# Optimization experiments

Hardware: AMD Instinct MI355X
Metric: run time of the kernel (lower is better)

Reference implementation:

```python
import jax, jax.numpy as jnp
import numpy as np

N, E = 65536, 524288
IN_DIM, HID_DIM, OUT_DIM = 1024, 512, 256


def setup_inputs() -> dict:
    key = jax.random.key(0)
    k1, k2, k3, k4, k5, k6 = jax.random.split(key, 6)
    h = jax.random.normal(k1, (N, IN_DIM), dtype=jnp.float32)
    src = jax.random.randint(k2, (E,), 0, N, dtype=jnp.int64)
    dst = jax.random.randint(k3, (E,), 0, N, dtype=jnp.int64)
    # Glorot-uniform weights as in DGL GraphConv
    lim1 = float(np.sqrt(6.0 / (IN_DIM + HID_DIM)))
    lim2 = float(np.sqrt(6.0 / (HID_DIM + OUT_DIM)))
    W1 = jax.random.uniform(k4, (IN_DIM, HID_DIM), jnp.float32, -lim1, lim1)
    W2 = jax.random.uniform(k5, (HID_DIM, OUT_DIM), jnp.float32, -lim2, lim2)
    b1 = jnp.zeros((HID_DIM,), jnp.float32)
    b2 = jnp.zeros((OUT_DIM,), jnp.float32)
    return {"h": h, "W1": W1, "b1": b1, "W2": W2, "b2": b2, "src": src, "dst": dst}


def _graph_conv(x, W, b, src, dst, inv_sqrt_dout, inv_sqrt_din):
    # DGL GraphConv, norm='both': D_in^{-1/2} A D_out^{-1/2} X W + b
    # Apply dense transform first (in_dim >= out_dim path in DGL) -- same math.
    x = x * inv_sqrt_dout[:, None]
    x = x @ W  # [N, out]
    agg = jax.ops.segment_sum(x[src], dst, num_segments=x.shape[0])  # scatter-add over edges
    return agg * inv_sqrt_din[:, None] + b


def reference(h, W1, b1, W2, b2, src, dst):
    n = h.shape[0]
    ones = jnp.ones((src.shape[0],), h.dtype)
    deg_out = jnp.maximum(jax.ops.segment_sum(ones, src, num_segments=n), 1.0)
    deg_in = jnp.maximum(jax.ops.segment_sum(ones, dst, num_segments=n), 1.0)
    inv_sqrt_dout = jax.lax.rsqrt(deg_out)
    inv_sqrt_din = jax.lax.rsqrt(deg_in)
    x = _graph_conv(h, W1, b1, src, dst, inv_sqrt_dout, inv_sqrt_din)
    x = jax.nn.elu(x)  # act; dropout p=0 -> identity
    out = _graph_conv(x, W2, b2, src, dst, inv_sqrt_dout, inv_sqrt_din)
    return out  # last_act = Identity
```

## Files before the change

### kernel.cpp

```cpp
#include <hip/hip_runtime.h>
#include <hip/hip_bf16.h>

#define IN_DIM 1024
#define HID 512
#define OUTD 256

typedef __attribute__((ext_vector_type(8))) short short8;
typedef __attribute__((ext_vector_type(4))) float f32x4;
typedef __attribute__((ext_vector_type(8))) unsigned short ushort8e;
typedef __attribute__((ext_vector_type(4))) unsigned short ushort4e;

template<int F> struct VecSel;
template<> struct VecSel<8> { using T = ushort8e; };
template<> struct VecSel<4> { using T = ushort4e; };


__device__ inline unsigned short f2bf(float f) {
    union { float f; unsigned u; } v; v.f = f;
    unsigned r = (v.u + 0x7FFF + ((v.u >> 16) & 1)) >> 16;
    return (unsigned short)r;
}

__device__ inline float bf2f(unsigned short u) {
    union { unsigned u; float f; } v; v.u = ((unsigned)u) << 16; return v.f;
}

__device__ inline void gload16(const void* g, void* l) {
    __builtin_amdgcn_global_load_lds(
        (const __attribute__((address_space(1))) void*)g,
        (__attribute__((address_space(3))) void*)l, 16, 0, 0);
}


__global__ void deg_kernel(const int* __restrict__ src, const int* __restrict__ dst,
                           int* __restrict__ dego, int* __restrict__ degi, int E) {
    int i = blockIdx.x * blockDim.x + threadIdx.x;
    if (i < E) {
        atomicAdd(&dego[src[i]], 1);
        atomicAdd(&degi[dst[i]], 1);
    }
}

__global__ void invsqrt_kernel(const int* __restrict__ dego, const int* __restrict__ degi,
                               float* __restrict__ iso, float* __restrict__ isi, int n) {
    int i = blockIdx.x * blockDim.x + threadIdx.x;
    if (i < n) {
        iso[i] = rsqrtf(fmaxf((float)dego[i], 1.0f));
        isi[i] = rsqrtf(fmaxf((float)degi[i], 1.0f));
    }
}


__global__ __launch_bounds__(256) void scan_block(const int* __restrict__ deg,
                                                  int* __restrict__ excl,
                                                  int* __restrict__ partials) {
    __shared__ int tmp[256];
    int tid = threadIdx.x;
    int i = blockIdx.x * 256 + tid;
    int v = deg[i];
    tmp[tid] = v;
    __syncthreads();
    #pragma unroll
    for (int off = 1; off < 256; off <<= 1) {
        int t = (tid >= off) ? tmp[tid - off] : 0;
        __syncthreads();
        tmp[tid] += t;
        __syncthreads();
    }
    excl[i] = tmp[tid] - v;
    if (tid == 255) partials[blockIdx.x] = tmp[255];
}

__global__ __launch_bounds__(256) void scan_partials(int* __restrict__ partials) {
    __shared__ int tmp[256];
    int tid = threadIdx.x;
    int v = partials[tid];
    tmp[tid] = v;
    __syncthreads();
    #pragma unroll
    for (int off = 1; off < 256; off <<= 1) {
        int t = (tid >= off) ? tmp[tid - off] : 0;
        __syncthreads();
        tmp[tid] += t;
        __syncthreads();
    }
    partials[tid] = tmp[tid] - v;
}

__global__ __launch_bounds__(256) void scan_add(const int* __restrict__ excl,
                                                const int* __restrict__ partials,
                                                const int* __restrict__ deg,
                                                int* __restrict__ row_start,
                                                int* __restrict__ cursor, int n) {
    int i = blockIdx.x * 256 + threadIdx.x;
    int v = excl[i] + partials[blockIdx.x];
    row_start[i] = v;
    cursor[i] = v;
    if (i == n - 1) row_start[n] = v + deg[i];
}

__global__ void csr_fill(const int* __restrict__ src, const int* __restrict__ dst,
                         int* __restrict__ cursor, int* __restrict__ eidx, int E) {
    int e = blockIdx.x * blockDim.x + threadIdx.x;
    if (e < E) {
        int pos = atomicAdd(&cursor[dst[e]], 1);
        eidx[pos] = src[e];
    }
}


__global__ void transpose_cvt(const float* __restrict__ W, unsigned short* __restrict__ Wt,
                              int K, int N) {
    int i = blockIdx.x * 256 + threadIdx.x;
    if (i < N * K) {
        int n = i / K, k = i - n * K;
        Wt[i] = f2bf(W[(size_t)k * N + n]);
    }
}


#define TM 128
#define TN 128
#define TK 64
#define NXCD 8

template<int AF32>
__global__ __launch_bounds__(256) void gemm_bf16_mfma(
    const void* __restrict__ Ap, const unsigned short* __restrict__ Bt,
    const float* __restrict__ rowscale, unsigned short* __restrict__ Cb,
    int M, int K, int Nc)
{
    __shared__ unsigned short As[2][TM][TK];
    __shared__ unsigned short Bs[2][TN][TK];

    const int tid  = threadIdx.x;
    const int lane = tid & 63;
    const int wave = tid >> 6;
    const int wr = wave >> 1, wc = wave & 1;
    const int lrow = lane & 15;
    const int lkg  = lane >> 4;

    const int nwg = gridDim.x;
    const int per = nwg / NXCD;
    const int lin = blockIdx.x;
    const int newlin = (lin % NXCD) * per + lin / NXCD;
    const int ncb = Nc / TN;
    const int m0 = (newlin / ncb) * TM;
    const int n0 = (newlin % ncb) * TN;

    int srow[4], sq[4];
    #pragma unroll
    for (int i = 0; i < 4; ++i) {
        int s = i * 256 + wave * 64 + lane;
        srow[i] = s >> 3;
        sq[i] = (s & 7) ^ ((s >> 3) & 7);
    }

    char* AsB = (char*)&As[0][0][0];
    char* BsB = (char*)&Bs[0][0][0];

    const float* Af = (const float*)Ap;
    const unsigned short* Ab = (const unsigned short*)Ap;

    auto stageOp = [&](const unsigned short* G, int rc0, int kt, char* opBase, int buf) {
        const int k0 = kt * TK;
        #pragma unroll
        for (int i = 0; i < 4; ++i)
            gload16(G + (size_t)(rc0 + srow[i]) * K + k0 + sq[i] * 8,
                    opBase + buf * 16384 + (i * 256 + wave * 64) * 16);
    };

    const int rA = tid >> 2;
    const int g  = tid & 3;
    const int qp0 = (2 * g) ^ (rA & 7);
    const int qp1 = (2 * g + 1) ^ (rA & 7);
    float sc0 = 1.f, sc1 = 1.f;
    if (AF32) {
        sc0 = rowscale[m0 + rA];
        sc1 = rowscale[m0 + rA + 64];
    }
    float4 L[8];
    auto loadA = [&](int kt) {
        const float* p0 = Af + (size_t)(m0 + rA) * K + kt * TK + g * 16;
        const float* p1 = p0 + (size_t)64 * K;
        L[0] = *reinterpret_cast<const float4*>(p0);
        L[1] = *reinterpret_cast<const float4*>(p0 + 4);
        L[2] = *reinterpret_cast<const float4*>(p0 + 8);
        L[3] = *reinterpret_cast<const float4*>(p0 + 12);
        L[4] = *reinterpret_cast<const float4*>(p1);
        L[5] = *reinterpret_cast<const float4*>(p1 + 4);
        L[6] = *reinterpret_cast<const float4*>(p1 + 8);
        L[7] = *reinterpret_cast<const float4*>(p1 + 12);
    };
    auto writeA = [&](int buf) {
        short8 k0v, k1v;
        #pragma unroll
        for (int r = 0; r < 2; ++r) {
            const float sc = r ? sc1 : sc0;
            const float4 f0 = L[r * 4 + 0], f1 = L[r * 4 + 1];
            const float4 f2 = L[r * 4 + 2], f3 = L[r * 4 + 3];
            k0v[0] = (short)f2bf(f0.x * sc); k0v[1] = (short)f2bf(f0.y * sc);
            k0v[2] = (short)f2bf(f0.z * sc); k0v[3] = (short)f2bf(f0.w * sc);
            k0v[4] = (short)f2bf(f1.x * sc); k0v[5] = (short)f2bf(f1.y * sc);
            k0v[6] = (short)f2bf(f1.z * sc); k0v[7] = (short)f2bf(f1.w * sc);
            k1v[0] = (short)f2bf(f2.x * sc); k1v[1] = (short)f2bf(f2.y * sc);
            k1v[2] = (short)f2bf(f2.z * sc); k1v[3] = (short)f2bf(f2.w * sc);
            k1v[4] = (short)f2bf(f3.x * sc); k1v[5] = (short)f2bf(f3.y * sc);
            k1v[6] = (short)f2bf(f3.z * sc); k1v[7] = (short)f2bf(f3.w * sc);
            char* rowb = AsB + buf * 16384 + (rA + r * 64) * 128;
            *reinterpret_cast<short8*>(rowb + qp0 * 16) = k0v;
            *reinterpret_cast<short8*>(rowb + qp1 * 16) = k1v;
        }
    };

    f32x4 acc[4][4] = {};

    stageOp(Bt, n0, 0, BsB, 0);
    if (AF32) { loadA(0); writeA(0); }
    else       stageOp(Ab, m0, 0, AsB, 0);
    __syncthreads();

    const int nk = K / TK;
    for (int kt = 0; kt < nk; ++kt) {
        const int cur = kt & 1, nxt = cur ^ 1;

        if (kt + 1 < nk) {
            stageOp(Bt, n0, kt + 1, BsB, nxt);
            if (AF32) loadA(kt + 1);
            else      stageOp(Ab, m0, kt + 1, AsB, nxt);
        }

        #pragma unroll
        for (int ks = 0; ks < 2; ++ks) {
            short8 af[4], bfr[4];
            #pragma unroll
            for (int mi = 0; mi < 4; ++mi) {
                const int row = wr * 64 + mi * 16 + lrow;
                const int qp = (ks * 4 + lkg) ^ (lrow & 7);
                af[mi] = *reinterpret_cast<const short8*>(&As[cur][row][qp * 8]);
            }
            #pragma unroll
            for (int ni = 0; ni < 4; ++ni) {
                const int row = wc * 64 + ni * 16 + lrow;
                const int qp = (ks * 4 + lkg) ^ (lrow & 7);
                bfr[ni] = *reinterpret_cast<const short8*>(&Bs[cur][row][qp * 8]);
            }
            #pragma unroll
            for (int mi = 0; mi < 4; ++mi)
                #pragma unroll
                for (int ni = 0; ni < 4; ++ni)
                    acc[mi][ni] = __builtin_amdgcn_mfma_f32_16x16x32_bf16(
                        af[mi], bfr[ni], acc[mi][ni], 0, 0, 0);
        }

        if (AF32 && kt + 1 < nk) writeA(nxt);

        __syncthreads();
    }

    #pragma unroll
    for (int mi = 0; mi < 4; ++mi)
        #pragma unroll
        for (int ni = 0; ni < 4; ++ni)
            #pragma unroll
            for (int r = 0; r < 4; ++r)
                Cb[(size_t)(m0 + wr * 64 + mi * 16 + (lane >> 4) * 4 + r) * Nc
                   + (n0 + wc * 64 + ni * 16 + lrow)] = f2bf(acc[mi][ni][r]);
}


template<int DIM, bool LAYER1>
__global__ __launch_bounds__(256) void aggregate(
    const int* __restrict__ row_start, const int* __restrict__ eidx,
    const unsigned short* __restrict__ Xb, const float* __restrict__ isi,
    const float* __restrict__ iso, const float* __restrict__ bias,
    unsigned short* __restrict__ out_bf, float* __restrict__ out_f)
{
    constexpr int F = DIM / 64;
    using VecT = typename VecSel<F>::T;
    const int node = blockIdx.x * 4 + (threadIdx.x >> 6);
    const int lane = threadIdx.x & 63;

    const int beg = row_start[node];
    const int end = row_start[node + 1];
    const unsigned short* base = Xb + lane * F;

    float acc[F] = {};
    int e = beg;
    for (; e + 1 < end; e += 2) {
        int i0 = eidx[e], i1 = eidx[e + 1];
        VecT v0 = *reinterpret_cast<const VecT*>(base + (size_t)i0 * DIM);
        VecT v1 = *reinterpret_cast<const VecT*>(base + (size_t)i1 * DIM);
        #pragma unroll
        for (int f = 0; f < F; ++f) { acc[f] += bf2f(v0[f]); acc[f] += bf2f(v1[f]); }
    }
    if (e < end) {
        VecT v0 = *reinterpret_cast<const VecT*>(base + (size_t)eidx[e] * DIM);
        #pragma unroll
        for (int f = 0; f < F; ++f) acc[f] += bf2f(v0[f]);
    }

    const float si = isi[node];
    float bv[F];
    #pragma unroll
    for (int q = 0; q < F / 4; ++q)
        *reinterpret_cast<float4*>(&bv[q * 4]) =
            *reinterpret_cast<const float4*>(bias + lane * F + q * 4);

    if (LAYER1) {
        const float so = iso[node];
        short8 o;
        #pragma unroll
        for (int f = 0; f < F; ++f) {
            float v = acc[f] * si + bv[f];
            v = v > 0.f ? v : expm1f(v);
            o[f] = (short)f2bf(v * so);
        }
        *reinterpret_cast<short8*>(out_bf + (size_t)node * DIM + lane * F) = o;
    } else {
        #pragma unroll
        for (int q = 0; q < F / 4; ++q) {
            float4 v = make_float4(acc[q * 4 + 0] * si + bv[q * 4 + 0],
                                   acc[q * 4 + 1] * si + bv[q * 4 + 1],
                                   acc[q * 4 + 2] * si + bv[q * 4 + 2],
                                   acc[q * 4 + 3] * si + bv[q * 4 + 3]);
            *reinterpret_cast<float4*>(out_f + (size_t)node * DIM + lane * F + q * 4) = v;
        }
    }
}


extern "C" void kernel_launch(void* const* d_in, const int* in_sizes, int n_in,
                              void* d_out, int out_size, void* d_ws, size_t ws_size,
                              hipStream_t stream) {
    const float* h  = (const float*)d_in[0];
    const float* W1 = (const float*)d_in[1];
    const float* b1 = (const float*)d_in[2];
    const float* W2 = (const float*)d_in[3];
    const float* b2 = (const float*)d_in[4];
    const int*   src = (const int*)d_in[5];
    const int*   dst = (const int*)d_in[6];

    const int N = in_sizes[0] / IN_DIM;
    const int E = in_sizes[5];
    float* out = (float*)d_out;

    int* dego      = (int*)d_ws;
    int* degi      = dego + N;
    int* excl      = degi + N;
    int* partials  = excl + N;
    int* row_start = partials + 256;
    int* cursor    = row_start + N + 64;
    int* eidx      = cursor + N;
    float* iso     = (float*)(eidx + E);
    float* isi     = iso + N;
    unsigned short* W1t = (unsigned short*)(isi + N);
    unsigned short* W2t = W1t + (size_t)IN_DIM * HID;
    unsigned short* X1b = W2t + (size_t)HID * OUTD;
    unsigned short* X2b = X1b;
    unsigned short* R2h = X1b + (size_t)N * HID;

    hipMemsetAsync(dego, 0, sizeof(int) * (size_t)2 * N, stream);

    deg_kernel<<<(E + 255) / 256, 256, 0, stream>>>(src, dst, dego, degi, E);
    invsqrt_kernel<<<(N + 255) / 256, 256, 0, stream>>>(dego, degi, iso, isi, N);

    scan_block<<<N / 256, 256, 0, stream>>>(degi, excl, partials);
    scan_partials<<<1, 256, 0, stream>>>(partials);
    scan_add<<<N / 256, 256, 0, stream>>>(excl, partials, degi, row_start, cursor, N);
    csr_fill<<<(E + 255) / 256, 256, 0, stream>>>(src, dst, cursor, eidx, E);

    transpose_cvt<<<(IN_DIM * HID + 255) / 256, 256, 0, stream>>>(W1, W1t, IN_DIM, HID);
    transpose_cvt<<<(HID * OUTD + 255) / 256, 256, 0, stream>>>(W2, W2t, HID, OUTD);

    gemm_bf16_mfma<1><<<(N / TM) * (HID / TN), 256, 0, stream>>>(
        h, W1t, iso, X1b, N, IN_DIM, HID);
    aggregate<HID, true><<<N / 4, 256, 0, stream>>>(
        row_start, eidx, X1b, isi, iso, b1, R2h, nullptr);

    gemm_bf16_mfma<0><<<(N / TM) * (OUTD / TN), 256, 0, stream>>>(
        R2h, W2t, nullptr, X2b, N, HID, OUTD);
    aggregate<OUTD, false><<<N / 4, 256, 0, stream>>>(
        row_start, eidx, X2b, isi, iso, b2, nullptr, out);
}
```

Before: 399.4 us.

## Move layer-1 out-degree scaling from GEMM A-load into edge aggregation

Stops scaling rows of h by inv_sqrt(deg_out) while converting A to bf16 inside the first GEMM. The aggregation kernel instead multiplies each gathered source row by that node's iso value. The change also replaces the manual per-element bf16 rounding with packed hardware conversion and unrolls the gather loop to four edges. This takes multiplies off the GEMM's conversion path, at the cost of an extra scalar gather per edge in aggregation. Rounding changes slightly because the scale is now applied after the bf16 GEMM rather than before it.

```diff
diff --git a/kernel.cpp b/kernel.cpp
--- a/kernel.cpp
+++ b/kernel.cpp
@@ -9,6 +9,7 @@
 typedef __attribute__((ext_vector_type(4))) float f32x4;
 typedef __attribute__((ext_vector_type(8))) unsigned short ushort8e;
 typedef __attribute__((ext_vector_type(4))) unsigned short ushort4e;
+typedef __attribute__((ext_vector_type(4))) unsigned int uint4e;
 
 template<int F> struct VecSel;
 template<> struct VecSel<8> { using T = ushort8e; };
@@ -23,6 +24,11 @@
 
 __device__ inline float bf2f(unsigned short u) {
     union { unsigned u; float f; } v; v.u = ((unsigned)u) << 16; return v.f;
+}
+
+__device__ inline unsigned pkbf(float a, float b) {
+    __hip_bfloat162 h = __float22bfloat162_rn(float2{a, b});
+    union { __hip_bfloat162 h; unsigned u; } v; v.h = h; return v.u;
 }
 
 __device__ inline void gload16(const void* g, void* l) {
@@ -127,8 +133,7 @@
 template<int AF32>
 __global__ __launch_bounds__(256) void gemm_bf16_mfma(
     const void* __restrict__ Ap, const unsigned short* __restrict__ Bt,
-    const float* __restrict__ rowscale, unsigned short* __restrict__ Cb,
-    int M, int K, int Nc)
+    unsigned short* __restrict__ Cb, int M, int K, int Nc)
 {
     __shared__ unsigned short As[2][TM][TK];
     __shared__ unsigned short Bs[2][TN][TK];
@@ -174,11 +179,6 @@
     const int g  = tid & 3;
     const int qp0 = (2 * g) ^ (rA & 7);
     const int qp1 = (2 * g + 1) ^ (rA & 7);
-    float sc0 = 1.f, sc1 = 1.f;
-    if (AF32) {
-        sc0 = rowscale[m0 + rA];
-        sc1 = rowscale[m0 + rA + 64];
-    }
     float4 L[8];
     auto loadA = [&](int kt) {
         const float* p0 = Af + (size_t)(m0 + rA) * K + kt * TK + g * 16;
@@ -193,23 +193,18 @@
         L[7] = *reinterpret_cast<const float4*>(p1 + 12);
     };
     auto writeA = [&](int buf) {
-        short8 k0v, k1v;
         #pragma unroll
         for (int r = 0; r < 2; ++r) {
-            const float sc = r ? sc1 : sc0;
             const float4 f0 = L[r * 4 + 0], f1 = L[r * 4 + 1];
             const float4 f2 = L[r * 4 + 2], f3 = L[r * 4 + 3];
-            k0v[0] = (short)f2bf(f0.x * sc); k0v[1] = (short)f2bf(f0.y * sc);
-            k0v[2] = (short)f2bf(f0.z * sc); k0v[3] = (short)f2bf(f0.w * sc);
-            k0v[4] = (short)f2bf(f1.x * sc); k0v[5] = (short)f2bf(f1.y * sc);
-            k0v[6] = (short)f2bf(f1.z * sc); k0v[7] = (short)f2bf(f1.w * sc);
-            k1v[0] = (short)f2bf(f2.x * sc); k1v[1] = (short)f2bf(f2.y * sc);
-            k1v[2] = (short)f2bf(f2.z * sc); k1v[3] = (short)f2bf(f2.w * sc);
-            k1v[4] = (short)f2bf(f3.x * sc); k1v[5] = (short)f2bf(f3.y * sc);
-            k1v[6] = (short)f2bf(f3.z * sc); k1v[7] = (short)f2bf(f3.w * sc);
+            uint4e a, b;
+            a[0] = pkbf(f0.x, f0.y); a[1] = pkbf(f0.z, f0.w);
+            a[2] = pkbf(f1.x, f1.y); a[3] = pkbf(f1.z, f1.w);
+            b[0] = pkbf(f2.x, f2.y); b[1] = pkbf(f2.z, f2.w);
+            b[2] = pkbf(f3.x, f3.y); b[3] = pkbf(f3.z, f3.w);
             char* rowb = AsB + buf * 16384 + (rA + r * 64) * 128;
-            *reinterpret_cast<short8*>(rowb + qp0 * 16) = k0v;
-            *reinterpret_cast<short8*>(rowb + qp1 * 16) = k1v;
+            *reinterpret_cast<uint4e*>(rowb + qp0 * 16) = a;
+            *reinterpret_cast<uint4e*>(rowb + qp1 * 16) = b;
         }
     };
 
@@ -264,7 +259,7 @@
         for (int ni = 0; ni < 4; ++ni)
             #pragma unroll
             for (int r = 0; r < 4; ++r)
-                Cb[(size_t)(m0 + wr * 64 + mi * 16 + (lane >> 4) * 4 + r) * Nc
+                Cb[(size_t)(m0 + wr * 64 + mi * 16 + lkg * 4 + r) * Nc
                    + (n0 + wc * 64 + ni * 16 + lrow)] = f2bf(acc[mi][ni][r]);
 }
 
@@ -287,17 +282,34 @@
 
     float acc[F] = {};
     int e = beg;
-    for (; e + 1 < end; e += 2) {
-        int i0 = eidx[e], i1 = eidx[e + 1];
+    for (; e + 3 < end; e += 4) {
+        int i0 = eidx[e], i1 = eidx[e + 1], i2 = eidx[e + 2], i3 = eidx[e + 3];
+        float s0 = 1.f, s1 = 1.f, s2 = 1.f, s3 = 1.f;
+        if (LAYER1) { s0 = iso[i0]; s1 = iso[i1]; s2 = iso[i2]; s3 = iso[i3]; }
         VecT v0 = *reinterpret_cast<const VecT*>(base + (size_t)i0 * DIM);
         VecT v1 = *reinterpret_cast<const VecT*>(base + (size_t)i1 * DIM);
-        #pragma unroll
-        for (int f = 0; f < F; ++f) { acc[f] += bf2f(v0[f]); acc[f] += bf2f(v1[f]); }
-    }
-    if (e < end) {
-        VecT v0 = *reinterpret_cast<const VecT*>(base + (size_t)eidx[e] * DIM);
-        #pragma unroll
-        for (int f = 0; f < F; ++f) acc[f] += bf2f(v0[f]);
+        VecT v2 = *reinterpret_cast<const VecT*>(base + (size_t)i2 * DIM);
+        VecT v3 = *reinterpret_cast<const VecT*>(base + (size_t)i3 * DIM);
+        #pragma unroll
+        for (int f = 0; f < F; ++f) {
+            if (LAYER1) {
+                acc[f] = fmaf(s0, bf2f(v0[f]), acc[f]);
+                acc[f] = fmaf(s1, bf2f(v1[f]), acc[f]);
+                acc[f] = fmaf(s2, bf2f(v2[f]), acc[f]);
+                acc[f] = fmaf(s3, bf2f(v3[f]), acc[f]);
+            } else {
+                acc[f] += bf2f(v0[f]); acc[f] += bf2f(v1[f]);
+                acc[f] += bf2f(v2[f]); acc[f] += bf2f(v3[f]);
+            }
+        }
+    }
+    for (; e < end; ++e) {
+        int i0 = eidx[e];
+        float s0 = LAYER1 ? iso[i0] : 1.f;
+        VecT v0 = *reinterpret_cast<const VecT*>(base + (size_t)i0 * DIM);
+        #pragma unroll
+        for (int f = 0; f < F; ++f)
+            acc[f] = LAYER1 ? fmaf(s0, bf2f(v0[f]), acc[f]) : acc[f] + bf2f(v0[f]);
     }
 
     const float si = isi[node];
@@ -374,12 +386,12 @@
     transpose_cvt<<<(HID * OUTD + 255) / 256, 256, 0, stream>>>(W2, W2t, HID, OUTD);
 
     gemm_bf16_mfma<1><<<(N / TM) * (HID / TN), 256, 0, stream>>>(
-        h, W1t, iso, X1b, N, IN_DIM, HID);
+        h, W1t, X1b, N, IN_DIM, HID);
     aggregate<HID, true><<<N / 4, 256, 0, stream>>>(
         row_start, eidx, X1b, isi, iso, b1, R2h, nullptr);
 
     gemm_bf16_mfma<0><<<(N / TM) * (OUTD / TN), 256, 0, stream>>>(
-        R2h, W2t, nullptr, X2b, N, HID, OUTD);
+        R2h, W2t, X2b, N, HID, OUTD);
     aggregate<OUTD, false><<<N / 4, 256, 0, stream>>>(
         row_start, eidx, X2b, isi, iso, b2, nullptr, out);
 }
```

After: 431.7 us. +8.1%, slower.
